# Performance work log

Measured on AMD Instinct MI355X. Metric: run time of the kernel, lower is better.

Reference implementation:

```python
import jax, jax.numpy as jnp
import numpy as np

N = 65536   # total nodes
B = 128     # graphs
G = 512     # nodes per graph
E = 65536   # directed edges (before BU flip + self loops)
IN = 512    # in_feats
HID = 64    # hid_feats
OUT = 64    # out_feats
H = 4       # heads (self.K)
NC = 4      # num_class


def _gat(x, src, dst, W, a_src, a_dst, bias, heads, out_ch, concat):
    # PyG GATConv: lin (no bias) -> per-edge LeakyReLU(0.2) attention logits ->
    # softmax over edges grouped by destination -> weighted sum -> +bias.
    n = x.shape[0]
    h = (x @ W).reshape(n, heads, out_ch)            # [N,H,C]
    asrc = (h * a_src).sum(-1)                       # [N,H]
    adst = (h * a_dst).sum(-1)                       # [N,H]
    e = jax.nn.leaky_relu(asrc[src] + adst[dst], 0.2)  # [Etot,H]
    m = jax.ops.segment_max(e, dst, num_segments=n)
    m = jnp.where(jnp.isfinite(m), m, 0.0)
    ex = jnp.exp(e - m[dst])
    den = jax.ops.segment_sum(ex, dst, num_segments=n)
    alpha = ex / den[dst]                            # self-loops guarantee den>0
    out = jax.ops.segment_sum(alpha[:, :, None] * h[src], dst, num_segments=n)
    out = out.reshape(n, heads * out_ch) if concat else out.mean(1)
    return out + bias


def _smean(v, seg, nseg):
    s = jax.ops.segment_sum(v, seg, num_segments=nseg)
    c = jax.ops.segment_sum(jnp.ones((v.shape[0], 1), v.dtype), seg, num_segments=nseg)
    return s / jnp.maximum(c, 1.0)


def setup_inputs() -> dict:
    key = jax.random.key(0)
    ks = jax.random.split(key, 24)
    x = jax.random.normal(ks[0], (N, IN), jnp.float32)
    root = jax.random.normal(ks[1], (B, IN), jnp.float32)
    # edges kept within each graph of G contiguous nodes (PyG batching layout)
    gid = jax.random.randint(ks[2], (E,), 0, B)
    src = gid * G + jax.random.randint(ks[3], (E,), 0, G)
    dst = gid * G + jax.random.randint(ks[4], (E,), 0, G)
    edge_index = jnp.stack([src, dst]).astype(jnp.int32)
    batch = jnp.repeat(jnp.arange(B, dtype=jnp.int32), G)
    ptr = jnp.arange(B + 1, dtype=jnp.int32) * G
    s = 0.05
    r = lambda i, shp: jax.random.normal(ks[i], shp, jnp.float32) * s
    return {
        'x': x, 'root': root, 'edge_index': edge_index, 'batch': batch, 'ptr': ptr,
        'W_post1': r(5, (IN, HID)), 'W_claim1': r(6, (IN, HID)),
        'W1': r(7, (2 * HID, H * HID)), 'att_src1': r(8, (H, HID)),
        'att_dst1': r(9, (H, HID)), 'b1': r(10, (H * HID,)),
        'W_post2': r(11, (HID, HID)), 'W_claim2': r(12, (IN, HID)),
        'W2': r(13, (8 * HID, H * OUT)), 'att_src2': r(14, (H, OUT)),
        'att_dst2': r(15, (H, OUT)), 'b2': r(16, (OUT,)),
        'W_fc': r(17, (4 * OUT, OUT)), 'b_fc': r(18, (OUT,)),
        'W_clf': r(19, (2 * OUT, NC)), 'b_clf': r(20, (NC,)),
    }


def reference(x, root, edge_index, batch, ptr,
              W_post1, W_claim1, W1, att_src1, att_dst1, b1,
              W_post2, W_claim2, W2, att_src2, att_dst2, b2,
              W_fc, b_fc, W_clf, b_clf):
    n = x.shape[0]
    nb = root.shape[0]
    # merged edges: TD + BU (flipped), then self loops (add_self_loops=True)
    merged = jnp.concatenate([edge_index, edge_index[::-1]], axis=1)
    loops = jnp.arange(n, dtype=edge_index.dtype)
    ei = jnp.concatenate([merged, jnp.stack([loops, loops])], axis=1)
    src, dst = ei[0], ei[1]
    # root broadcast (replaces per-batch python loop)
    root_extend = root[batch]                         # [N,IN]
    # PostLevelAttention: gated fusion of node feats and root feats
    h_x = x @ W_post1
    h_c = root_extend @ W_claim1
    g = jax.nn.sigmoid(h_x + h_c)
    h1 = jnp.concatenate([g * h_x + (1 - g) * h_c, h_x], -1)   # [N,2*HID]
    x2 = _gat(h1, src, dst, W1, att_src1, att_dst1, b1, H, HID, True)  # [N,4*HID]
    xr = jax.nn.relu(x2)
    # PostLevelAttention2 on each of the K=4 head slices (vectorized over k)
    hs = jnp.einsum('nkh,hd->nkd', xr.reshape(n, H, HID), W_post2)  # [N,4,HID]
    hc2 = (root_extend @ W_claim2)[:, None, :]                      # [N,1,HID]
    g2 = jax.nn.sigmoid(hs + hc2)
    x3 = jnp.concatenate([g2 * hs + (1 - g2) * hc2, hs], -1).reshape(n, 8 * HID)
    x4 = _gat(x3, src, dst, W2, att_src2, att_dst2, b2, H, OUT, False)  # [N,OUT]
    xr2 = jax.nn.relu(x4)
    # root embedding per graph (x[ptr[i]]) broadcast back to nodes
    h_c3 = xr2[ptr[:-1]][batch]                        # [N,OUT]
    h_joint = jnp.concatenate([h_c3, xr2, xr2 * h_c3, jnp.abs(h_c3 - xr2)], 1)
    beta = jax.nn.softmax(jnp.tanh(h_joint @ W_fc + b_fc), axis=-1)
    s_hat = _smean(beta * xr2, batch, nb)
    s = _smean(xr2, batch, nb)
    logits = jnp.concatenate([s_hat, s], 1) @ W_clf + b_clf
    return jax.nn.log_softmax(logits, axis=1)
```

## Files before the change

### kernel.cpp

```cpp
#include <hip/hip_runtime.h>
#include <math.h>

#define NN   65536
#define BB   128
#define GGR  512
#define EE   65536
#define INF_ 512
#define HIDD 64

typedef __attribute__((ext_vector_type(8))) short bf16x8;
typedef __attribute__((ext_vector_type(4))) float f32x4;
typedef unsigned short ushort_t;
typedef unsigned int uint_t;

static __device__ __forceinline__ float sigmoidf_(float x){ return 1.0f/(1.0f+__expf(-x)); }
static __device__ __forceinline__ float lrelu_(float x){ return x>=0.0f ? x : 0.2f*x; }
static __device__ __forceinline__ float tanhf_(float x){
  float e = __expf(2.f*x);
  return 1.f - 2.f/(e + 1.f);
}

static __device__ __forceinline__ ushort_t f2b(float f){
  union { float f; uint_t u; } v; v.f = f;
  uint_t u = v.u;
  uint_t r = (u + 0x7fffu + ((u >> 16) & 1u)) >> 16;
  return (ushort_t)r;
}
static __device__ __forceinline__ float b2f(uint_t u16){
  union { uint_t u; float f; } v; v.u = u16 << 16; return v.f;
}

static __device__ __forceinline__ void gld16(const void* g, void* l){
  __builtin_amdgcn_global_load_lds((const __attribute__((address_space(1))) void*)g,
                                   (__attribute__((address_space(3))) void*)l, 16, 0, 0);
}

__global__ void k_prep(const float* __restrict__ W1, const float* __restrict__ W2,
                       const float* __restrict__ Wp1, const float* __restrict__ Wp2,
                       const float* __restrict__ Wfc,
                       ushort_t* __restrict__ W1t, ushort_t* __restrict__ W2t,
                       ushort_t* __restrict__ Wp1t, ushort_t* __restrict__ Wp2t,
                       ushort_t* __restrict__ Wfct,
                       const float* __restrict__ root, const float* __restrict__ Wc1,
                       const float* __restrict__ Wc2, float* __restrict__ hc1,
                       float* __restrict__ hc2){
  if (blockIdx.x >= 832){
    int b = blockIdx.x - 832;
    int f = threadIdx.x;
    if (f < 64){
      const float* r = root + (size_t)b*INF_;
      float a1 = 0.f, a2 = 0.f;
      for (int k = 0; k < INF_; ++k){
        float rv = r[k];
        a1 = fmaf(rv, Wc1[k*HIDD+f], a1);
        a2 = fmaf(rv, Wc2[k*HIDD+f], a2);
      }
      hc1[b*HIDD+f] = a1; hc2[b*HIDD+f] = a2;
    }
    return;
  }
  int idx = blockIdx.x*256 + threadIdx.x;
  if (idx < 32768){
    int k = idx >> 8, c = idx & 255;
    W1t[(size_t)c*128 + k] = f2b(W1[idx]);
  } else if (idx < 163840){
    int j = idx - 32768; int k = j >> 8, c = j & 255;
    W2t[(size_t)c*512 + k] = f2b(W2[j]);
  } else if (idx < 196608){
    int j = idx - 163840; int k = j >> 6, c = j & 63;
    Wp1t[(size_t)c*512 + k] = f2b(Wp1[j]);
  } else if (idx < 200704){
    int j = idx - 196608; int k = j >> 6, c = j & 63;
    Wp2t[(size_t)c*64 + k] = f2b(Wp2[j]);
  } else if (idx < 212992){
    int j = idx - 200704; int k = j >> 6, c = j & 63;
    Wfct[(size_t)c*192 + k] = f2b(Wfc[4096 + j]);
  }
}

__global__ __launch_bounds__(256) void k_l1(
    const float* __restrict__ x,
    const ushort_t* __restrict__ Wp1t,
    const float* __restrict__ hc1,
    const ushort_t* __restrict__ W1t,
    const float* __restrict__ att_s, const float* __restrict__ att_d,
    ushort_t* __restrict__ Hout,
    float* __restrict__ asrc, float* __restrict__ adst){
  __shared__ __align__(16) float xs[64*128];
  __shared__ __align__(16) ushort_t h1s[64*128];
  int tid = threadIdx.x;
  int w = tid >> 6, lane = tid & 63;
  int lr = lane & 15, lk = lane >> 4;
  int n0 = blockIdx.x * 64;
  int g = n0 >> 9;
  int sw = (lr & 7) << 4;
  f32x4 accA[4];
  #pragma unroll
  for (int ci = 0; ci < 4; ++ci) accA[ci] = (f32x4){0.f,0.f,0.f,0.f};
  const char* xg = (const char*)(x + (size_t)n0*512);
  char* Ls = (char*)xs;
  const ushort_t* BbA = Wp1t + (size_t)lr*512 + lk*8;
  int rl = w*16 + lr;
  for (int s = 0; s < 4; ++s){
    #pragma unroll
    for (int i = 0; i < 8; ++i){
      int p = i*4096 + tid*16;
      int row = p >> 9;
      int l = p ^ ((row & 7) << 4);
      gld16(xg + (size_t)row*2048 + s*512 + (l & 511), Ls + p);
    }
    __syncthreads();
    #pragma unroll
    for (int k0 = 0; k0 < 128; k0 += 32){
      int lg = rl*512 + (k0 + lk*8)*4;
      float4 fa = *(const float4*)(Ls + (lg ^ sw));
      float4 fb = *(const float4*)(Ls + ((lg + 16) ^ sw));
      bf16x8 af;
      af[0]=(short)f2b(fa.x); af[1]=(short)f2b(fa.y); af[2]=(short)f2b(fa.z); af[3]=(short)f2b(fa.w);
      af[4]=(short)f2b(fb.x); af[5]=(short)f2b(fb.y); af[6]=(short)f2b(fb.z); af[7]=(short)f2b(fb.w);
      #pragma unroll
      for (int ci = 0; ci < 4; ++ci){
        bf16x8 bfv = *(const bf16x8*)(BbA + (size_t)ci*16*512 + s*128 + k0);
        accA[ci] = __builtin_amdgcn_mfma_f32_16x16x32_bf16(af, bfv, accA[ci], 0, 0, 0);
      }
    }
    __syncthreads();
  }
  char* Hc = (char*)h1s;
  #pragma unroll
  for (int ci = 0; ci < 4; ++ci){
    int col = ci*16 + lr;
    float hc = hc1[g*64 + col];
    #pragma unroll
    for (int q = 0; q < 4; ++q){
      int row = w*16 + lk*4 + q;
      int swr = (row & 7) << 4;
      float hx = accA[ci][q];
      float gg = sigmoidf_(hx + hc);
      float fo = gg*hx + (1.f-gg)*hc;
      *(ushort_t*)(Hc + ((row*256 + col*2) ^ swr))        = f2b(fo);
      *(ushort_t*)(Hc + ((row*256 + (64 + col)*2) ^ swr)) = f2b(hx);
    }
  }
  __syncthreads();
  int c0 = w * 64;
  f32x4 acc[4][4];
  #pragma unroll
  for (int ri = 0; ri < 4; ++ri)
    #pragma unroll
    for (int ci = 0; ci < 4; ++ci) acc[ri][ci] = (f32x4){0.f,0.f,0.f,0.f};
  #pragma unroll
  for (int k0 = 0; k0 < 128; k0 += 32){
    bf16x8 af[4], bfv[4];
    #pragma unroll
    for (int ri = 0; ri < 4; ++ri){
      int lg = (ri*16 + lr)*256 + (k0 + lk*8)*2;
      af[ri] = *(const bf16x8*)(Hc + (lg ^ sw));
    }
    #pragma unroll
    for (int ci = 0; ci < 4; ++ci)
      bfv[ci] = *(const bf16x8*)(W1t + (size_t)(c0 + ci*16 + lr)*128 + k0 + lk*8);
    #pragma unroll
    for (int ri = 0; ri < 4; ++ri)
      #pragma unroll
      for (int ci = 0; ci < 4; ++ci)
        acc[ri][ci] = __builtin_amdgcn_mfma_f32_16x16x32_bf16(af[ri], bfv[ci], acc[ri][ci], 0, 0, 0);
  }
  float as_[4], ad_[4];
  #pragma unroll
  for (int ci = 0; ci < 4; ++ci){
    as_[ci] = att_s[c0 + ci*16 + lr];
    ad_[ci] = att_d[c0 + ci*16 + lr];
  }
  #pragma unroll
  for (int ri = 0; ri < 4; ++ri){
    #pragma unroll
    for (int q = 0; q < 4; ++q){
      int row = n0 + ri*16 + lk*4 + q;
      float ps = 0.f, pd = 0.f;
      #pragma unroll
      for (int ci = 0; ci < 4; ++ci){
        float v = acc[ri][ci][q];
        Hout[(size_t)row*256 + c0 + ci*16 + lr] = f2b(v);
        ps = fmaf(v, as_[ci], ps);
        pd = fmaf(v, ad_[ci], pd);
      }
      #pragma unroll
      for (int m = 1; m < 16; m <<= 1){
        ps += __shfl_xor(ps, m);
        pd += __shfl_xor(pd, m);
      }
      if (lr == 0){
        asrc[(size_t)row*4 + w] = ps;
        adst[(size_t)row*4 + w] = pd;
      }
    }
  }
}

__global__ __launch_bounds__(256) void k_l2(
    const ushort_t* __restrict__ xrb,
    const ushort_t* __restrict__ Wp2t,
    const float* __restrict__ hc2,
    const ushort_t* __restrict__ W2t,
    const float* __restrict__ att_s, const float* __restrict__ att_d,
    ushort_t* __restrict__ Hout,
    float* __restrict__ asrc, float* __restrict__ adst){
  __shared__ __align__(16) ushort_t xs[64*256];
  __shared__ __align__(16) ushort_t x3s[64*128];
  int tid = threadIdx.x;
  int w = tid >> 6, lane = tid & 63;
  int lr = lane & 15, lk = lane >> 4;
  int n0 = blockIdx.x * 64;
  int g = n0 >> 9;
  int sw = (lr & 7) << 4;
  char* Xc = (char*)xs;
  char* Sc = (char*)x3s;
  {
    const char* Ag = (const char*)(xrb + (size_t)n0*256);
    #pragma unroll
    for (int i = 0; i < 8; ++i){
      int p = i*4096 + tid*16;
      int row = p >> 9;
      int l = p ^ ((row & 7) << 4);
      gld16(Ag + (size_t)row*512 + (l & 511), Xc + p);
    }
  }
  __syncthreads();
  int c0 = w * 64;
  f32x4 acc[4][4];
  #pragma unroll
  for (int ri = 0; ri < 4; ++ri)
    #pragma unroll
    for (int ci = 0; ci < 4; ++ci) acc[ri][ci] = (f32x4){0.f,0.f,0.f,0.f};
  for (int hd = 0; hd < 4; ++hd){
    f32x4 acc2[4];
    #pragma unroll
    for (int ci = 0; ci < 4; ++ci) acc2[ci] = (f32x4){0.f,0.f,0.f,0.f};
    #pragma unroll
    for (int k0 = 0; k0 < 64; k0 += 32){
      int lg = (w*16 + lr)*512 + (hd*64 + k0 + lk*8)*2;
      bf16x8 af = *(const bf16x8*)(Xc + (lg ^ sw));
      #pragma unroll
      for (int ci = 0; ci < 4; ++ci){
        bf16x8 bfv = *(const bf16x8*)(Wp2t + (size_t)(ci*16 + lr)*64 + k0 + lk*8);
        acc2[ci] = __builtin_amdgcn_mfma_f32_16x16x32_bf16(af, bfv, acc2[ci], 0, 0, 0);
      }
    }
    #pragma unroll
    for (int ci = 0; ci < 4; ++ci){
      int col = ci*16 + lr;
      float hc = hc2[g*64 + col];
      #pragma unroll
      for (int q = 0; q < 4; ++q){
        int row = w*16 + lk*4 + q;
        int swr = (row & 7) << 4;
        float a = acc2[ci][q];
        float gg = sigmoidf_(a + hc);
        *(ushort_t*)(Sc + ((row*256 + col*2) ^ swr))        = f2b(gg*a + (1.f-gg)*hc);
        *(ushort_t*)(Sc + ((row*256 + (64 + col)*2) ^ swr)) = f2b(a);
      }
    }
    __syncthreads();
    #pragma unroll
    for (int k0 = 0; k0 < 128; k0 += 32){
      bf16x8 af[4], bfv[4];
      #pragma unroll
      for (int ri = 0; ri < 4; ++ri){
        int lg = (ri*16 + lr)*256 + (k0 + lk*8)*2;
        af[ri] = *(const bf16x8*)(Sc + (lg ^ sw));
      }
      #pragma unroll
      for (int ci = 0; ci < 4; ++ci)
        bfv[ci] = *(const bf16x8*)(W2t + (size_t)(c0 + ci*16 + lr)*512 + hd*128 + k0 + lk*8);
      #pragma unroll
      for (int ri = 0; ri < 4; ++ri)
        #pragma unroll
        for (int ci = 0; ci < 4; ++ci)
          acc[ri][ci] = __builtin_amdgcn_mfma_f32_16x16x32_bf16(af[ri], bfv[ci], acc[ri][ci], 0, 0, 0);
    }
    if (hd < 3) __syncthreads();
  }
  float as_[4], ad_[4];
  #pragma unroll
  for (int ci = 0; ci < 4; ++ci){
    as_[ci] = att_s[c0 + ci*16 + lr];
    ad_[ci] = att_d[c0 + ci*16 + lr];
  }
  #pragma unroll
  for (int ri = 0; ri < 4; ++ri){
    #pragma unroll
    for (int q = 0; q < 4; ++q){
      int row = n0 + ri*16 + lk*4 + q;
      float ps = 0.f, pd = 0.f;
      #pragma unroll
      for (int ci = 0; ci < 4; ++ci){
        float v = acc[ri][ci][q];
        Hout[(size_t)row*256 + c0 + ci*16 + lr] = f2b(v);
        ps = fmaf(v, as_[ci], ps);
        pd = fmaf(v, ad_[ci], pd);
      }
      #pragma unroll
      for (int m = 1; m < 16; m <<= 1){
        ps += __shfl_xor(ps, m);
        pd += __shfl_xor(pd, m);
      }
      if (lr == 0){
        asrc[(size_t)row*4 + w] = ps;
        adst[(size_t)row*4 + w] = pd;
      }
    }
  }
}

__global__ void k_count(const int* __restrict__ ei, int* __restrict__ deg){
  int t = blockIdx.x*256 + threadIdx.x;
  int s = ei[t], d = ei[EE + t];
  atomicAdd(&deg[d], 1);
  atomicAdd(&deg[s], 1);
}

__global__ void k_scan1(const int* __restrict__ deg, int* __restrict__ offa,
                        int* __restrict__ bsum){
  __shared__ int sm[256];
  int tid = threadIdx.x, idx = blockIdx.x*256 + tid;
  int v = deg[idx] + 1;
  sm[tid] = v; __syncthreads();
  for (int o = 1; o < 256; o <<= 1){
    int t = (tid >= o) ? sm[tid-o] : 0;
    __syncthreads();
    sm[tid] += t;
    __syncthreads();
  }
  offa[idx] = sm[tid] - v;
  if (tid == 255) bsum[blockIdx.x] = sm[255];
}

__global__ void k_scan2(int* __restrict__ bsum){
  __shared__ int sm[256];
  int tid = threadIdx.x;
  int v = bsum[tid];
  sm[tid] = v; __syncthreads();
  for (int o = 1; o < 256; o <<= 1){
    int t = (tid >= o) ? sm[tid-o] : 0;
    __syncthreads();
    sm[tid] += t;
    __syncthreads();
  }
  bsum[tid] = sm[tid] - v;
}

__global__ void k_scan3(int* __restrict__ offa, const int* __restrict__ bsum){
  int idx = blockIdx.x*256 + threadIdx.x;
  offa[idx] += bsum[idx >> 8];
}

__global__ void k_fill(const int* __restrict__ ei, const int* __restrict__ offa,
                       int* __restrict__ cur, int* __restrict__ elist){
  int t = blockIdx.x*256 + threadIdx.x;
  int s = ei[t], d = ei[EE + t];
  int p = atomicAdd(&cur[d], 1); elist[offa[d] + p] = s;
  p = atomicAdd(&cur[s], 1);     elist[offa[s] + p] = d;
  p = atomicAdd(&cur[t], 1);     elist[offa[t] + p] = t;
}

template<int LAYER>
__global__ __launch_bounds__(256) void k_agg(const int* __restrict__ offa,
                                             const int* __restrict__ deg,
                                             const int* __restrict__ elist,
                                             const ushort_t* __restrict__ h,
                                             const float* __restrict__ asrc,
                                             const float* __restrict__ adst,
                                             const float* __restrict__ bias,
                                             ushort_t* __restrict__ outb,
                                             float* __restrict__ outf){
  __shared__ float eS[4][4][17][4];
  __shared__ int   sS[4][4][17];
  int bid = blockIdx.x;
  int swz = (bid & 7) * (4096/8) + (bid >> 3);
  int tid = threadIdx.x;
  int wave = tid >> 6, lane = tid & 63;
  int grp = lane >> 4, l = lane & 15;
  int n = swz*16 + wave*4 + grp;
  int o0 = offa[n], cnt = deg[n] + 1;
  float4 adv = *(const float4*)&adst[(size_t)n*4];
  float ad[4] = {adv.x, adv.y, adv.z, adv.w};
  int lim = (cnt < 16) ? cnt : 16;
  int s_l = elist[o0 + ((l < cnt) ? l : 0)];
  float4 asv = *(const float4*)&asrc[(size_t)s_l*4];
  float e_l[4];
  e_l[0] = lrelu_(asv.x + ad[0]); e_l[1] = lrelu_(asv.y + ad[1]);
  e_l[2] = lrelu_(asv.z + ad[2]); e_l[3] = lrelu_(asv.w + ad[3]);
  if (l < lim){
    sS[wave][grp][l] = s_l;
    *(float4*)&eS[wave][grp][l][0] = make_float4(e_l[0], e_l[1], e_l[2], e_l[3]);
  }
  float m[4];
  #pragma unroll
  for (int hh = 0; hh < 4; ++hh) m[hh] = (l < cnt) ? e_l[hh] : -1e30f;
  for (int i = 16 + l; i < cnt; i += 16){
    int s = elist[o0 + i];
    float4 a2 = *(const float4*)&asrc[(size_t)s*4];
    m[0] = fmaxf(m[0], lrelu_(a2.x + ad[0]));
    m[1] = fmaxf(m[1], lrelu_(a2.y + ad[1]));
    m[2] = fmaxf(m[2], lrelu_(a2.z + ad[2]));
    m[3] = fmaxf(m[3], lrelu_(a2.w + ad[3]));
  }
  #pragma unroll
  for (int mask = 1; mask < 16; mask <<= 1)
    #pragma unroll
    for (int hh = 0; hh < 4; ++hh) m[hh] = fmaxf(m[hh], __shfl_xor(m[hh], mask));
  int myh = l >> 2;
  float mm = m[myh];
  float den = 0.f;
  float accv[16] = {};
  for (int i = 0; i < lim; ++i){
    int s = sS[wave][grp][i];
    float e = eS[wave][grp][i][myh];
    float ex = __expf(e - mm);
    den += ex;
    const uint4* hp = (const uint4*)(h + (size_t)s*256 + l*16);
    uint4 h0 = hp[0], h1v = hp[1];
    uint_t uu[8] = {h0.x, h0.y, h0.z, h0.w, h1v.x, h1v.y, h1v.z, h1v.w};
    #pragma unroll
    for (int r = 0; r < 8; ++r){
      accv[2*r+0] = fmaf(ex, b2f(uu[r] & 0xffffu), accv[2*r+0]);
      accv[2*r+1] = fmaf(ex, b2f(uu[r] >> 16),     accv[2*r+1]);
    }
  }
  for (int i = 16; i < cnt; ++i){
    int s = elist[o0 + i];
    float4 a2 = *(const float4*)&asrc[(size_t)s*4];
    float e = lrelu_(((const float*)&a2)[myh] + ad[myh]);
    float ex = __expf(e - mm);
    den += ex;
    const uint4* hp = (const uint4*)(h + (size_t)s*256 + l*16);
    uint4 h0 = hp[0], h1v = hp[1];
    uint_t uu[8] = {h0.x, h0.y, h0.z, h0.w, h1v.x, h1v.y, h1v.z, h1v.w};
    #pragma unroll
    for (int r = 0; r < 8; ++r){
      accv[2*r+0] = fmaf(ex, b2f(uu[r] & 0xffffu), accv[2*r+0]);
      accv[2*r+1] = fmaf(ex, b2f(uu[r] >> 16),     accv[2*r+1]);
    }
  }
  float inv = 1.0f / den;
  if (LAYER == 1){
    #pragma unroll
    for (int r = 0; r < 4; ++r){
      int c = l*16 + r*4;
      float4 bv = *(const float4*)&bias[c];
      float o0v = fmaxf(accv[r*4+0]*inv + bv.x, 0.f);
      float o1v = fmaxf(accv[r*4+1]*inv + bv.y, 0.f);
      float o2v = fmaxf(accv[r*4+2]*inv + bv.z, 0.f);
      float o3v = fmaxf(accv[r*4+3]*inv + bv.w, 0.f);
      uint2 pk;
      pk.x = (uint_t)f2b(o0v) | ((uint_t)f2b(o1v) << 16);
      pk.y = (uint_t)f2b(o2v) | ((uint_t)f2b(o3v) << 16);
      *(uint2*)&outb[(size_t)n*256 + c] = pk;
    }
  } else {
    #pragma unroll
    for (int r = 0; r < 16; ++r) accv[r] *= inv;
    #pragma unroll
    for (int r = 0; r < 16; ++r){
      accv[r] += __shfl_xor(accv[r], 4);
      accv[r] += __shfl_xor(accv[r], 8);
    }
    if (l < 4){
      #pragma unroll
      for (int r = 0; r < 4; ++r){
        int c = l*16 + r*4;
        float4 bv = *(const float4*)&bias[c];
        float4 o;
        o.x = fmaxf(accv[r*4+0]*0.25f + bv.x, 0.f);
        o.y = fmaxf(accv[r*4+1]*0.25f + bv.y, 0.f);
        o.z = fmaxf(accv[r*4+2]*0.25f + bv.z, 0.f);
        o.w = fmaxf(accv[r*4+3]*0.25f + bv.w, 0.f);
        *(float4*)&outf[(size_t)n*64 + c] = o;
      }
    }
  }
}

__global__ __launch_bounds__(256) void k_pool_mfma(
    const float* __restrict__ xr2,
    const ushort_t* __restrict__ Wfct,
    const float* __restrict__ Wfc,
    const float* __restrict__ bfc,
    float* __restrict__ shat,
    float* __restrict__ ssum){
  __shared__ __align__(16) float xs[64][68];
  __shared__ float rls[64];
  __shared__ float bs[64];
  __shared__ float ls_sh[64];
  __shared__ float ls_s[64];
  int tid = threadIdx.x;
  int n0 = blockIdx.x * 64;
  int g = n0 >> 9;
  {
    int row = tid >> 4, col4 = (tid & 15) * 4;
    #pragma unroll
    for (int i = 0; i < 4; ++i){
      float4 v = *(const float4*)&xr2[(size_t)(n0 + row + i*16)*64 + col4];
      *(float4*)&xs[row + i*16][col4] = v;
    }
    if (tid < 16){
      float4 v = *(const float4*)&xr2[(size_t)((size_t)g*GGR)*64 + tid*4];
      *(float4*)&rls[tid*4] = v;
    }
    if (tid >= 128 && tid < 192){ ls_sh[tid-128] = 0.f; ls_s[tid-128] = 0.f; }
  }
  __syncthreads();
  if (tid < 64){
    float b = bfc[tid];
    for (int j = 0; j < 64; ++j) b = fmaf(rls[j], Wfc[j*64 + tid], b);
    bs[tid] = b;
  }
  __syncthreads();
  int w = tid >> 6, lane = tid & 63;
  int lr = lane & 15, lk = lane >> 4;
  f32x4 acc[4];
  #pragma unroll
  for (int ci = 0; ci < 4; ++ci) acc[ci] = (f32x4){0.f,0.f,0.f,0.f};
  int arow = w*16 + lr;
  #pragma unroll
  for (int k0 = 0; k0 < 192; k0 += 32){
    int seg = k0 >> 6;
    int cb = (k0 & 63) + lk*8;
    bf16x8 af;
    #pragma unroll
    for (int j = 0; j < 8; ++j){
      float xv = xs[arow][cb + j];
      float rv = rls[cb + j];
      float v = (seg == 0) ? xv : (seg == 1 ? xv*rv : fabsf(rv - xv));
      af[j] = (short)f2b(v);
    }
    #pragma unroll
    for (int ci = 0; ci < 4; ++ci){
      bf16x8 bfv = *(const bf16x8*)(Wfct + (size_t)(ci*16+lr)*192 + k0 + lk*8);
      acc[ci] = __builtin_amdgcn_mfma_f32_16x16x32_bf16(af, bfv, acc[ci], 0, 0, 0);
    }
  }
  float bsv[4];
  #pragma unroll
  for (int ci = 0; ci < 4; ++ci) bsv[ci] = bs[ci*16 + lr];
  float c_sh[4] = {0.f,0.f,0.f,0.f}, c_s[4] = {0.f,0.f,0.f,0.f};
  #pragma unroll
  for (int q = 0; q < 4; ++q){
    int rrow = w*16 + lk*4 + q;
    float t[4];
    float mx = -1e30f;
    #pragma unroll
    for (int ci = 0; ci < 4; ++ci){
      t[ci] = tanhf_(acc[ci][q] + bsv[ci]);
      mx = fmaxf(mx, t[ci]);
    }
    #pragma unroll
    for (int mask = 1; mask < 16; mask <<= 1) mx = fmaxf(mx, __shfl_xor(mx, mask));
    float e[4], s = 0.f;
    #pragma unroll
    for (int ci = 0; ci < 4; ++ci){ e[ci] = __expf(t[ci] - mx); s += e[ci]; }
    #pragma unroll
    for (int mask = 1; mask < 16; mask <<= 1) s += __shfl_xor(s, mask);
    float invs = 1.0f / s;
    #pragma unroll
    for (int ci = 0; ci < 4; ++ci){
      float xv = xs[rrow][ci*16 + lr];
      c_sh[ci] = fmaf(e[ci]*invs, xv, c_sh[ci]);
      c_s[ci] += xv;
    }
  }
  #pragma unroll
  for (int ci = 0; ci < 4; ++ci){
    c_sh[ci] += __shfl_xor(c_sh[ci], 16); c_sh[ci] += __shfl_xor(c_sh[ci], 32);
    c_s[ci]  += __shfl_xor(c_s[ci], 16);  c_s[ci]  += __shfl_xor(c_s[ci], 32);
  }
  if (lk == 0){
    #pragma unroll
    for (int ci = 0; ci < 4; ++ci){
      atomicAdd(&ls_sh[ci*16 + lr], c_sh[ci]);
      atomicAdd(&ls_s[ci*16 + lr], c_s[ci]);
    }
  }
  __syncthreads();
  if (tid < 64){
    atomicAdd(&shat[g*64 + tid], ls_sh[tid]);
    atomicAdd(&ssum[g*64 + tid], ls_s[tid]);
  }
}

__global__ void k_final(const float* __restrict__ shat, const float* __restrict__ ssum,
                        const float* __restrict__ Wc, const float* __restrict__ bc,
                        float* __restrict__ outp){
  int g = threadIdx.x;
  float l0 = bc[0], l1 = bc[1], l2 = bc[2], l3 = bc[3];
  const float s512 = 1.0f/512.0f;
  for (int j = 0; j < 64; ++j){
    float sh = shat[g*64 + j]*s512;
    float ss = ssum[g*64 + j]*s512;
    float4 w1 = *(const float4*)&Wc[j*4];
    float4 w2 = *(const float4*)&Wc[(64+j)*4];
    l0 = fmaf(sh, w1.x, fmaf(ss, w2.x, l0));
    l1 = fmaf(sh, w1.y, fmaf(ss, w2.y, l1));
    l2 = fmaf(sh, w1.z, fmaf(ss, w2.z, l2));
    l3 = fmaf(sh, w1.w, fmaf(ss, w2.w, l3));
  }
  float mx = fmaxf(fmaxf(l0,l1), fmaxf(l2,l3));
  float s = __expf(l0-mx)+__expf(l1-mx)+__expf(l2-mx)+__expf(l3-mx);
  float lse = mx + logf(s);
  outp[g*4+0] = l0 - lse;
  outp[g*4+1] = l1 - lse;
  outp[g*4+2] = l2 - lse;
  outp[g*4+3] = l3 - lse;
}

extern "C" void kernel_launch(void* const* d_in, const int* in_sizes, int n_in,
                              void* d_out, int out_size, void* d_ws, size_t ws_size,
                              hipStream_t stream){
  const float* x        = (const float*)d_in[0];
  const float* root     = (const float*)d_in[1];
  const int*   ei       = (const int*)d_in[2];
  const float* W_post1  = (const float*)d_in[5];
  const float* W_claim1 = (const float*)d_in[6];
  const float* W1       = (const float*)d_in[7];
  const float* att_src1 = (const float*)d_in[8];
  const float* att_dst1 = (const float*)d_in[9];
  const float* b1       = (const float*)d_in[10];
  const float* W_post2  = (const float*)d_in[11];
  const float* W_claim2 = (const float*)d_in[12];
  const float* W2       = (const float*)d_in[13];
  const float* att_src2 = (const float*)d_in[14];
  const float* att_dst2 = (const float*)d_in[15];
  const float* b2       = (const float*)d_in[16];
  const float* W_fc     = (const float*)d_in[17];
  const float* b_fc     = (const float*)d_in[18];
  const float* W_clf    = (const float*)d_in[19];
  const float* b_clf    = (const float*)d_in[20];
  float* out = (float*)d_out;

  char* w = (char*)d_ws;
  size_t o = 0;
  auto alloc = [&](size_t bytes)->char*{ char* p = w + o; o += (bytes + 255) & ~(size_t)255; return p; };
  ushort_t* RB   = (ushort_t*)alloc((size_t)NN*256*2);
  ushort_t* xrb  = (ushort_t*)alloc((size_t)NN*256*2);
  float* xr2  = (float*)alloc((size_t)NN*64*4);
  float* asrc = (float*)alloc((size_t)NN*4*4);
  float* adst = (float*)alloc((size_t)NN*4*4);
  float* hc1  = (float*)alloc(128*64*4);
  float* hc2  = (float*)alloc(128*64*4);
  ushort_t* W1t  = (ushort_t*)alloc((size_t)256*128*2);
  ushort_t* W2t  = (ushort_t*)alloc((size_t)256*512*2);
  ushort_t* Wp1t = (ushort_t*)alloc((size_t)64*512*2);
  ushort_t* Wp2t = (ushort_t*)alloc((size_t)64*64*2);
  ushort_t* Wfct = (ushort_t*)alloc((size_t)64*192*2);
  int*   deg  = (int*)alloc((size_t)NN*4);
  int*   cur  = (int*)alloc((size_t)NN*4);
  int*   offa = (int*)alloc((size_t)NN*4);
  int*   bsum = (int*)alloc(256*4);
  int*   elist= (int*)alloc((size_t)(2*EE+NN)*4);
  float* shat = (float*)alloc(128*64*4);
  float* ssumv= (float*)alloc(128*64*4);

  ushort_t* h2b = RB;
  ushort_t* h3b = RB;

  hipMemsetAsync(deg,  0, (size_t)NN*8, stream);
  hipMemsetAsync(shat, 0, 2*128*64*4, stream);

  k_prep<<<960, 256, 0, stream>>>(W1, W2, W_post1, W_post2, W_fc,
                                  W1t, W2t, Wp1t, Wp2t, Wfct,
                                  root, W_claim1, W_claim2, hc1, hc2);
  k_count<<<256, 256, 0, stream>>>(ei, deg);
  k_scan1<<<256, 256, 0, stream>>>(deg, offa, bsum);
  k_scan2<<<1, 256, 0, stream>>>(bsum);
  k_scan3<<<256, 256, 0, stream>>>(offa, bsum);
  k_fill<<<256, 256, 0, stream>>>(ei, offa, cur, elist);
  k_l1<<<1024, 256, 0, stream>>>(x, Wp1t, hc1, W1t, att_src1, att_dst1, h2b, asrc, adst);
  k_agg<1><<<4096, 256, 0, stream>>>(offa, deg, elist, h2b, asrc, adst, b1, xrb, nullptr);
  k_l2<<<1024, 256, 0, stream>>>(xrb, Wp2t, hc2, W2t, att_src2, att_dst2, h3b, asrc, adst);
  k_agg<2><<<4096, 256, 0, stream>>>(offa, deg, elist, h3b, asrc, adst, b2, nullptr, xr2);
  k_pool_mfma<<<1024, 256, 0, stream>>>(xr2, Wfct, W_fc, b_fc, shat, ssumv);
  k_final<<<1, 128, 0, stream>>>(shat, ssumv, W_clf, b_clf, out);
  (void)in_sizes; (void)n_in; (void)out_size; (void)ws_size;
}
```

Baseline: 263.8 us.

## Double-buffer x tile loads in layer-1 GEMM to overlap global loads with MFMA

Splits the K loop of the first projection into 8 stages of 64 columns and double-buffers the x tiles in shared memory. The next stage is issued before computing on the current one, with partial vmcnt waits, so global-load latency overlaps the MFMA work. Total LDS stays at 32KB because the h1 staging buffer now reuses the first buffer. The cost is more barriers per tile and reliance on hand-written waitcnt and barrier ordering, which could be fragile.

Result: no change. 261.2 us (-1.0%).

```diff
diff --git a/kernel.cpp b/kernel.cpp
--- a/kernel.cpp
+++ b/kernel.cpp
@@ -86,47 +86,61 @@
     const float* __restrict__ att_s, const float* __restrict__ att_d,
     ushort_t* __restrict__ Hout,
     float* __restrict__ asrc, float* __restrict__ adst){
-  __shared__ __align__(16) float xs[64*128];
-  __shared__ __align__(16) ushort_t h1s[64*128];
+  __shared__ __align__(16) char Lds[32768];
   int tid = threadIdx.x;
   int w = tid >> 6, lane = tid & 63;
   int lr = lane & 15, lk = lane >> 4;
   int n0 = blockIdx.x * 64;
   int g = n0 >> 9;
   int sw = (lr & 7) << 4;
+  const char* xg = (const char*)(x + (size_t)n0*512);
+  char* buf0 = Lds;
+  char* buf1 = Lds + 16384;
+  auto STAGE = [&](char* dst, int s){
+    #pragma unroll
+    for (int i = 0; i < 4; ++i){
+      int p = i*4096 + tid*16;
+      int row = p >> 8;
+      int l = p ^ ((row & 7) << 4);
+      gld16(xg + (size_t)row*2048 + s*256 + (l & 255), dst + p);
+    }
+  };
   f32x4 accA[4];
   #pragma unroll
   for (int ci = 0; ci < 4; ++ci) accA[ci] = (f32x4){0.f,0.f,0.f,0.f};
-  const char* xg = (const char*)(x + (size_t)n0*512);
-  char* Ls = (char*)xs;
   const ushort_t* BbA = Wp1t + (size_t)lr*512 + lk*8;
   int rl = w*16 + lr;
-  for (int s = 0; s < 4; ++s){
-    #pragma unroll
-    for (int i = 0; i < 8; ++i){
-      int p = i*4096 + tid*16;
-      int row = p >> 9;
-      int l = p ^ ((row & 7) << 4);
-      gld16(xg + (size_t)row*2048 + s*512 + (l & 511), Ls + p);
-    }
-    __syncthreads();
-    #pragma unroll
-    for (int k0 = 0; k0 < 128; k0 += 32){
-      int lg = rl*512 + (k0 + lk*8)*4;
-      float4 fa = *(const float4*)(Ls + (lg ^ sw));
-      float4 fb = *(const float4*)(Ls + ((lg + 16) ^ sw));
+  STAGE(buf0, 0);
+  #pragma unroll
+  for (int s = 0; s < 8; ++s){
+    char* cur = (s & 1) ? buf1 : buf0;
+    if (s < 7){
+      char* nxt = (s & 1) ? buf0 : buf1;
+      STAGE(nxt, s + 1);
+      asm volatile("s_waitcnt vmcnt(4)" ::: "memory");
+    } else {
+      asm volatile("s_waitcnt vmcnt(0)" ::: "memory");
+    }
+    __builtin_amdgcn_s_barrier();
+    asm volatile("" ::: "memory");
+    #pragma unroll
+    for (int k0 = 0; k0 < 64; k0 += 32){
+      int lg = rl*256 + (k0 + lk*8)*4;
+      float4 fa = *(const float4*)(cur + (lg ^ sw));
+      float4 fb = *(const float4*)(cur + ((lg + 16) ^ sw));
       bf16x8 af;
       af[0]=(short)f2b(fa.x); af[1]=(short)f2b(fa.y); af[2]=(short)f2b(fa.z); af[3]=(short)f2b(fa.w);
       af[4]=(short)f2b(fb.x); af[5]=(short)f2b(fb.y); af[6]=(short)f2b(fb.z); af[7]=(short)f2b(fb.w);
       #pragma unroll
       for (int ci = 0; ci < 4; ++ci){
-        bf16x8 bfv = *(const bf16x8*)(BbA + (size_t)ci*16*512 + s*128 + k0);
+        bf16x8 bfv = *(const bf16x8*)(BbA + (size_t)ci*16*512 + s*64 + k0);
         accA[ci] = __builtin_amdgcn_mfma_f32_16x16x32_bf16(af, bfv, accA[ci], 0, 0, 0);
       }
     }
-    __syncthreads();
-  }
-  char* Hc = (char*)h1s;
+    asm volatile("" ::: "memory");
+    __builtin_amdgcn_s_barrier();
+  }
+  char* Hc = buf0;
   #pragma unroll
   for (int ci = 0; ci < 4; ++ci){
     int col = ci*16 + lr;
```

## Convert x to bf16 in registers and stage per-wave full-K tiles in LDS

Applied to the files above, without the earlier changes.

Each wave now loads its own 16 rows of x with direct float4 global loads, converts them to bf16 once, and writes the whole 512-wide K slab into a 64KB swizzled LDS buffer. The four-stage loop of async global-to-LDS copies with block-wide barriers is gone. The MFMA loop then reads bf16 fragments straight from LDS with no per-fragment conversion. The cost is a larger LDS footprint (64KB per block), which can lower occupancy, and the global loads are no longer asynchronous LDS fills.

Measured after the change: 256.8 us. -2.6%, faster.

```diff
diff --git a/kernel.cpp b/kernel.cpp
--- a/kernel.cpp
+++ b/kernel.cpp
@@ -86,47 +86,41 @@
     const float* __restrict__ att_s, const float* __restrict__ att_d,
     ushort_t* __restrict__ Hout,
     float* __restrict__ asrc, float* __restrict__ adst){
-  __shared__ __align__(16) float xs[64*128];
-  __shared__ __align__(16) ushort_t h1s[64*128];
+  __shared__ __align__(16) char Lds[65536];
   int tid = threadIdx.x;
   int w = tid >> 6, lane = tid & 63;
   int lr = lane & 15, lk = lane >> 4;
   int n0 = blockIdx.x * 64;
   int g = n0 >> 9;
   int sw = (lr & 7) << 4;
+  char* chunk = Lds + w*16384;
+  const char* xg = (const char*)(x + (size_t)(n0 + w*16)*512);
+  #pragma unroll
+  for (int it = 0; it < 32; ++it){
+    int b = it*1024 + lane*16;
+    float4 v = *(const float4*)(xg + b);
+    int row = b >> 11;
+    int off = (b & 2047) >> 1;
+    uint2 pk;
+    pk.x = (uint_t)f2b(v.x) | ((uint_t)f2b(v.y) << 16);
+    pk.y = (uint_t)f2b(v.z) | ((uint_t)f2b(v.w) << 16);
+    *(uint2*)(chunk + ((row*1024 + off) ^ ((row & 7) << 4))) = pk;
+  }
   f32x4 accA[4];
   #pragma unroll
   for (int ci = 0; ci < 4; ++ci) accA[ci] = (f32x4){0.f,0.f,0.f,0.f};
-  const char* xg = (const char*)(x + (size_t)n0*512);
-  char* Ls = (char*)xs;
   const ushort_t* BbA = Wp1t + (size_t)lr*512 + lk*8;
-  int rl = w*16 + lr;
-  for (int s = 0; s < 4; ++s){
-    #pragma unroll
-    for (int i = 0; i < 8; ++i){
-      int p = i*4096 + tid*16;
-      int row = p >> 9;
-      int l = p ^ ((row & 7) << 4);
-      gld16(xg + (size_t)row*2048 + s*512 + (l & 511), Ls + p);
-    }
-    __syncthreads();
-    #pragma unroll
-    for (int k0 = 0; k0 < 128; k0 += 32){
-      int lg = rl*512 + (k0 + lk*8)*4;
-      float4 fa = *(const float4*)(Ls + (lg ^ sw));
-      float4 fb = *(const float4*)(Ls + ((lg + 16) ^ sw));
-      bf16x8 af;
-      af[0]=(short)f2b(fa.x); af[1]=(short)f2b(fa.y); af[2]=(short)f2b(fa.z); af[3]=(short)f2b(fa.w);
-      af[4]=(short)f2b(fb.x); af[5]=(short)f2b(fb.y); af[6]=(short)f2b(fb.z); af[7]=(short)f2b(fb.w);
-      #pragma unroll
-      for (int ci = 0; ci < 4; ++ci){
-        bf16x8 bfv = *(const bf16x8*)(BbA + (size_t)ci*16*512 + s*128 + k0);
-        accA[ci] = __builtin_amdgcn_mfma_f32_16x16x32_bf16(af, bfv, accA[ci], 0, 0, 0);
-      }
-    }
-    __syncthreads();
-  }
-  char* Hc = (char*)h1s;
+  #pragma unroll
+  for (int k0 = 0; k0 < 512; k0 += 32){
+    bf16x8 af = *(const bf16x8*)(chunk + ((lr*1024 + (k0 + lk*8)*2) ^ sw));
+    #pragma unroll
+    for (int ci = 0; ci < 4; ++ci){
+      bf16x8 bfv = *(const bf16x8*)(BbA + (size_t)ci*16*512 + k0);
+      accA[ci] = __builtin_amdgcn_mfma_f32_16x16x32_bf16(af, bfv, accA[ci], 0, 0, 0);
+    }
+  }
+  __syncthreads();
+  char* Hc = Lds;
   #pragma unroll
   for (int ci = 0; ci < 4; ++ci){
     int col = ci*16 + lr;
```
